# Kernel tuning notes

Hardware: AMD Instinct MI355X
Metric: run time of the kernel (lower is better)

## Reference

```python
import jax, jax.numpy as jnp
import numpy as np

SOS = 4998
EOS = 4999
SCALING = 2.0


def setup_inputs() -> dict:
    key = jax.random.key(0)
    ks = jax.random.split(key, 12)
    B, T, E, D, A, C, F, ODIM, L = 32, 1000, 512, 1024, 512, 10, 100, 5000, 100
    s = 0.02
    return {
        "hpad": jax.random.normal(ks[0], (B, T, E), jnp.float32),
        "ys": jax.random.randint(ks[1], (B, L), 0, SOS, jnp.int32),
        # AttLoc params
        "w_enc": jax.random.normal(ks[2], (A, E), jnp.float32) * s,
        "b_enc": jnp.zeros((A,), jnp.float32),
        "w_dec": jax.random.normal(ks[3], (A, D), jnp.float32) * s,
        "w_att": jax.random.normal(ks[4], (A, C), jnp.float32) * s,
        "w_conv": jax.random.normal(ks[5], (C, 1, 2 * F + 1), jnp.float32) * s,  # OIH 1D conv kernel
        "w_gvec": jax.random.normal(ks[6], (1, A), jnp.float32) * s,
        "b_gvec": jnp.zeros((1,), jnp.float32),
        # Decoder params
        "embed": jax.random.normal(ks[7], (ODIM, D), jnp.float32) * s,
        "w_ih": jax.random.normal(ks[8], (4 * D, D + E), jnp.float32) * s,
        "w_hh": jax.random.normal(ks[9], (4 * D, D), jnp.float32) * s,
        "b_ih": jnp.zeros((4 * D,), jnp.float32),
        "b_hh": jnp.zeros((4 * D,), jnp.float32),
        "w_out": jax.random.normal(ks[10], (ODIM, D), jnp.float32) * s,
        "b_out": jnp.zeros((ODIM,), jnp.float32),
    }


def _decode(hpad, ys, w_enc, b_enc, w_dec, w_att, w_conv, w_gvec, b_gvec,
            embed, w_ih, w_hh, b_ih, b_hh, w_out, b_out):
    B, T, E = hpad.shape
    D = w_hh.shape[1]
    F = (w_conv.shape[-1] - 1) // 2
    # ys_in = [sos; y] per utterance (all same length -> already padded)
    ys_in = jnp.concatenate([jnp.full((B, 1), SOS, ys.dtype), ys], axis=1)  # [B, olen]
    eys = embed[ys_in]                                                      # [B, olen, D]
    # pre_compute_enc_h = mlp_enc(enc_h)
    pre = jnp.einsum('bte,ae->bta', hpad, w_enc) + b_enc                    # [B, T, A]
    att0 = jnp.full((B, T), 1.0 / T, hpad.dtype)   # uniform init attention (all hlen == T)
    z0 = jnp.zeros((B, D), hpad.dtype)
    c0 = jnp.zeros((B, D), hpad.dtype)

    def step(carry, ey_i):
        z, c, aw = carry
        # location-aware conv over previous attention weights: [B,1,T] -> [B,C,T]
        conv = jax.lax.conv_general_dilated(aw[:, None, :], w_conv, (1,), [(F, F)],
                                            dimension_numbers=('NCH', 'OIH', 'NCH'))
        att_feat = jnp.einsum('bct,ac->bta', conv, w_att)                   # mlp_att
        dec = (z @ w_dec.T)[:, None, :]                                     # mlp_dec, tiled
        e = jnp.tanh(att_feat + pre + dec) @ w_gvec[0] + b_gvec[0]          # [B, T]
        w = jax.nn.softmax(SCALING * e, axis=1)
        ctx = jnp.einsum('bt,bte->be', w, hpad)                             # [B, E]
        # LSTMCell
        x = jnp.concatenate([ey_i, ctx], axis=1)                            # [B, D+E]
        gates = x @ w_ih.T + b_ih + z @ w_hh.T + b_hh
        i_g, f_g, g_g, o_g = jnp.split(gates, 4, axis=1)
        c_new = jax.nn.sigmoid(f_g) * c + jax.nn.sigmoid(i_g) * jnp.tanh(g_g)
        z_new = jax.nn.sigmoid(o_g) * jnp.tanh(c_new)
        return (z_new, c_new, w), z_new

    _, z_all = jax.lax.scan(step, (z0, c0, att0), jnp.swapaxes(eys, 0, 1))  # [olen, B, D]
    y_all = jnp.einsum('obd,vd->obv', z_all, w_out) + b_out                 # [olen, B, odim]
    return jnp.swapaxes(y_all, 0, 1)                                        # [B, olen, odim]


def reference(hpad, ys, w_enc, b_enc, w_dec, w_att, w_conv, w_gvec, b_gvec,
              embed, w_ih, w_hh, b_ih, b_hh, w_out, b_out):
    return _decode(hpad, ys, w_enc, b_enc, w_dec, w_att, w_conv, w_gvec, b_gvec,
                   embed, w_ih, w_hh, b_ih, b_hh, w_out, b_out)
```

## Files before the change

kernel.cpp:

```cpp
#include <hip/hip_runtime.h>
#include <math.h>

#define B_    32
#define T_    1000
#define E_    512
#define D_    1024
#define A_    512
#define C_    10
#define F_    100
#define ODIM_ 5000
#define OLEN_ 101
#define SOS_  4998

#define OFF_PRE   0u
#define N_PREF    (32u*512u*1000u/2u)
#define OFF_HPB   (OFF_PRE + N_PREF)
#define N_HPBF    (32u*1000u*512u/2u)
#define OFF_DEC   (OFF_HPB + N_HPBF)
#define N_DEC     (32u*512u)
#define OFF_CONV  (OFF_DEC + N_DEC)
#define N_CONVB   (32u*10u*1000u)
#define OFF_AW    (OFF_CONV + N_CONVB)
#define N_AW      (32u*1000u)
#define OFF_S     (OFF_AW + N_AW)
#define N_S       (64u)
#define OFF_CTX   (OFF_S + N_S)
#define N_CTX     (32u*512u)
#define OFF_GP    (OFF_CTX + N_CTX)
#define N_GP      (8u*32u*4096u)
#define OFF_Z     (OFF_GP + N_GP)
#define N_Z       (32u*1024u)
#define OFF_C     (OFF_Z + N_Z)
#define OFF_ZALL  (OFF_C + N_Z)

__device__ __forceinline__ float fast_tanh(float x) {
    float cx = fminf(8.f, fmaxf(-8.f, x));
    float e = __expf(2.f * cx);
    return (e - 1.f) * __builtin_amdgcn_rcpf(e + 1.f);
}
__device__ __forceinline__ float fast_sigmoid(float x) {
    float cx = fminf(30.f, fmaxf(-30.f, x));
    return __builtin_amdgcn_rcpf(1.f + __expf(-cx));
}

__device__ __forceinline__ unsigned bf16rne(float f) {
    unsigned u = __float_as_uint(f);
    return (u + 0x7fffu + ((u >> 16) & 1u)) >> 16;
}
__device__ __forceinline__ unsigned packbf(float lo, float hi) {
    return bf16rne(lo) | (bf16rne(hi) << 16);
}
__device__ __forceinline__ float bflo(unsigned u) { return __uint_as_float(u << 16); }
__device__ __forceinline__ float bfhi(unsigned u) { return __uint_as_float(u & 0xffff0000u); }

__global__ __launch_bounds__(256) void k_init(float* ws) {
    int i = blockIdx.x * 256 + threadIdx.x;
    if (i < (int)N_Z) { ws[OFF_Z + i] = 0.f; ws[OFF_C + i] = 0.f; }
    if (i < (int)N_CTX) ws[OFF_CTX + i] = 0.f;
    if (i < (int)N_AW) ws[OFF_AW + i] = 1.0f;
    if (i < 64) ws[OFF_S + i] = (i >= 32) ? 1000.f : 0.f;
}

__global__ __launch_bounds__(256) void k_hp16(const float* __restrict__ hp, float* ws) {
    uint2* hpb = (uint2*)(ws + OFF_HPB);
    const float4* src = (const float4*)hp;
    for (unsigned i = blockIdx.x * 256 + threadIdx.x; i < 4096000u; i += 4000u * 256u) {
        float4 v = src[i];
        uint2 o;
        o.x = packbf(v.x, v.y);
        o.y = packbf(v.z, v.w);
        hpb[i] = o;
    }
}

__global__ __launch_bounds__(256) void k_pre_t(const float* __restrict__ hp,
                                               const float* __restrict__ we,
                                               const float* __restrict__ be,
                                               float* ws) {
    __shared__ float As[64][68];
    __shared__ float Bs[64][68];
    unsigned short* preb = (unsigned short*)(ws + OFF_PRE);
    int bt = blockIdx.y;
    int b = bt >> 4, tc = bt & 15;
    int t0 = tc * 64;
    int n0 = blockIdx.x * 64;
    int tid = threadIdx.x;
    int tr = tid >> 4, tcl = tid & 15;
    float acc[4][4] = {};
    for (int k0 = 0; k0 < 512; k0 += 64) {
        for (int i = tid; i < 1024; i += 256) {
            int m = i >> 4, kq = (i & 15) << 2;
            int t = t0 + m;
            float4 v = (t < 1000) ? *(const float4*)&hp[((size_t)(b * 1000 + t)) * 512 + k0 + kq]
                                  : make_float4(0.f, 0.f, 0.f, 0.f);
            As[kq + 0][m] = v.x; As[kq + 1][m] = v.y; As[kq + 2][m] = v.z; As[kq + 3][m] = v.w;
            float4 w = *(const float4*)&we[(size_t)(n0 + m) * 512 + k0 + kq];
            Bs[kq + 0][m] = w.x; Bs[kq + 1][m] = w.y; Bs[kq + 2][m] = w.z; Bs[kq + 3][m] = w.w;
        }
        __syncthreads();
        #pragma unroll 16
        for (int kk = 0; kk < 64; ++kk) {
            float4 av = *(const float4*)&As[kk][tr << 2];
            float4 bv = *(const float4*)&Bs[kk][tcl << 2];
            float a[4] = {av.x, av.y, av.z, av.w};
            float bq[4] = {bv.x, bv.y, bv.z, bv.w};
            #pragma unroll
            for (int i = 0; i < 4; i++)
                #pragma unroll
                for (int j = 0; j < 4; j++) acc[i][j] += a[i] * bq[j];
        }
        __syncthreads();
    }
    int tt = t0 + (tr << 2);
    if (tt < 1000) {
        #pragma unroll
        for (int j = 0; j < 4; ++j) {
            int a = n0 + (tcl << 2) + j;
            float bea = be[a];
            uint2 o;
            o.x = packbf(acc[0][j] + bea, acc[1][j] + bea);
            o.y = packbf(acc[2][j] + bea, acc[3][j] + bea);
            *(uint2*)&preb[((size_t)(b * 512 + a)) * 1000 + tt] = o;
        }
    }
}

__global__ __launch_bounds__(256, 2) void k_prep(const float* __restrict__ wdec,
                                                 const float* __restrict__ wconv,
                                                 const float* __restrict__ wih,
                                                 const float* __restrict__ whh,
                                                 const float* __restrict__ embed,
                                                 const int* __restrict__ ys,
                                                 float* ws, int step) {
    int tid = threadIdx.x;
    if (blockIdx.x < 1024) {
        int u = blockIdx.x;
        if (u < 64) ws[OFF_CTX + u * 256 + tid] = 0.f;
        if (u == 64 && tid < 32) ws[OFF_S + (step & 1) * 32 + tid] = 0.f;
        int w = u * 4 + (tid >> 6);
        int lane = tid & 63;
        int a = w >> 3, bg7 = w & 7;
        const float4* wr = (const float4*)(wdec + (size_t)a * 1024);
        float4 w4[4];
        #pragma unroll
        for (int i = 0; i < 4; i++) w4[i] = wr[i * 64 + lane];
        float acc[4] = {0.f, 0.f, 0.f, 0.f};
        #pragma unroll
        for (int bb = 0; bb < 4; ++bb) {
            const float4* zr = (const float4*)(ws + OFF_Z + (size_t)(bg7 * 4 + bb) * 1024);
            #pragma unroll
            for (int i = 0; i < 4; i++) {
                float4 z4 = zr[i * 64 + lane];
                acc[bb] += w4[i].x * z4.x + w4[i].y * z4.y + w4[i].z * z4.z + w4[i].w * z4.w;
            }
        }
        #pragma unroll
        for (int off = 32; off > 0; off >>= 1) {
            acc[0] += __shfl_xor(acc[0], off, 64);
            acc[1] += __shfl_xor(acc[1], off, 64);
            acc[2] += __shfl_xor(acc[2], off, 64);
            acc[3] += __shfl_xor(acc[3], off, 64);
        }
        if (lane == 0) {
            #pragma unroll
            for (int bb = 0; bb < 4; ++bb)
                ws[OFF_DEC + (bg7 * 4 + bb) * 512 + a] = acc[bb];
        }
    } else if (blockIdx.x < 1344) {
        int blk = blockIdx.x - 1024;
        int b = blk / 10, c = blk - b * 10;
        if (tid >= 250) return;
        float invS = __builtin_amdgcn_rcpf(ws[OFF_S + ((step + 1) & 1) * 32 + b]);
        int t = tid * 4;
        const float* ar = ws + OFF_AW + b * 1000;
        const float* wc = wconv + c * 201;
        float a0, a1, a2, a3;
        a0 = (t - 100 >= 0) ? ar[t - 100] : 0.f;
        a1 = (t -  99 >= 0) ? ar[t -  99] : 0.f;
        a2 = (t -  98 >= 0) ? ar[t -  98] : 0.f;
        a3 = (t -  97 >= 0) ? ar[t -  97] : 0.f;
        float c0 = 0.f, c1 = 0.f, c2 = 0.f, c3 = 0.f;
        #pragma unroll 4
        for (int j = 0; j < 201; ++j) {
            float w = wc[j];
            c0 += a0 * w; c1 += a1 * w; c2 += a2 * w; c3 += a3 * w;
            a0 = a1; a1 = a2; a2 = a3;
            int ni = t + j - 96;
            a3 = (ni >= 0 && ni < 1000) ? ar[ni] : 0.f;
        }
        float* o = ws + OFF_CONV + (size_t)(b * 10 + c) * 1000 + t;
        o[0] = c0 * invS; o[1] = c1 * invS; o[2] = c2 * invS; o[3] = c3 * invS;
    } else {
        __shared__ float wlds[32][132];
        __shared__ float xs[32][36];
        int blk = blockIdx.x - 1344;
        int nt = blk & 31, ks = blk >> 5;
        int n0 = nt * 128;
        bool isE = (ks < 4);
        int kloc = isE ? ks * 256 : (ks - 4) * 256;
        int r = tid >> 1, h = tid & 1;
        int bx = tid >> 3, q8 = tid & 7;
        int tok = (step == 0) ? SOS_ : ys[bx * 100 + step - 1];
        const float* xsrc = isE ? (embed + (size_t)tok * 1024 + kloc)
                                : (ws + OFF_Z + (size_t)bx * 1024 + kloc);
        int nq = tid & 31, bq = tid >> 5;
        float acc[4][4] = {};
        for (int kc = 0; kc < 8; ++kc) {
            int koff = kc * 32;
            {
                const float* wrow = isE ? (wih + (size_t)(n0 + r) * 1536 + kloc + koff + h * 16)
                                        : (whh + (size_t)(n0 + r) * 1024 + kloc + koff + h * 16);
                #pragma unroll
                for (int j = 0; j < 4; ++j) {
                    float4 v = *(const float4*)&wrow[j * 4];
                    int kb = h * 16 + j * 4;
                    wlds[kb + 0][r] = v.x; wlds[kb + 1][r] = v.y;
                    wlds[kb + 2][r] = v.z; wlds[kb + 3][r] = v.w;
                }
            }
            {
                float4 v = *(const float4*)&xsrc[koff + q8 * 4];
                xs[q8 * 4 + 0][bx] = v.x; xs[q8 * 4 + 1][bx] = v.y;
                xs[q8 * 4 + 2][bx] = v.z; xs[q8 * 4 + 3][bx] = v.w;
            }
            __syncthreads();
            #pragma unroll 8
            for (int kk = 0; kk < 32; ++kk) {
                float4 wv = *(const float4*)&wlds[kk][nq * 4];
                float4 xv = *(const float4*)&xs[kk][bq * 4];
                float wa[4] = {wv.x, wv.y, wv.z, wv.w};
                float xa[4] = {xv.x, xv.y, xv.z, xv.w};
                #pragma unroll
                for (int i = 0; i < 4; i++)
                    #pragma unroll
                    for (int j = 0; j < 4; j++) acc[i][j] += wa[i] * xa[j];
            }
            __syncthreads();
        }
        float* gp = ws + OFF_GP + (size_t)(ks * 32 + bq * 4) * 4096 + n0 + nq * 4;
        #pragma unroll
        for (int j = 0; j < 4; j++)
            #pragma unroll
            for (int i = 0; i < 4; i++)
                gp[(size_t)j * 4096 + i] = acc[i][j];
    }
}

__global__ __launch_bounds__(512, 2) void k_ectx(const float* __restrict__ watt,
                                                 const float* __restrict__ gvec,
                                                 const float* __restrict__ bgv,
                                                 float* ws, int step) {
    __shared__ float sa[512 * 12];
    __shared__ float part[1024];
    __shared__ float wsh[128];
    const unsigned short* preb = (const unsigned short*)(ws + OFF_PRE);
    const unsigned short* hpb  = (const unsigned short*)(ws + OFF_HPB);
    int b = blockIdx.x >> 3, tc = blockIdx.x & 7;
    int tbase = tc * 128;
    int tid = threadIdx.x;
    {
        const float* wrow = watt + tid * 10;
        float* d = sa + tid * 12;
        #pragma unroll
        for (int c = 0; c < 10; ++c) d[c] = wrow[c];
        d[10] = gvec[tid];
        d[11] = ws[OFF_DEC + b * 512 + tid];
    }
    __syncthreads();
    int w = tid >> 6, l = tid & 63;
    int t = tbase + l * 2;
    bool valid = (t < 1000);
    float2 cvv[10];
    const float* convb = ws + OFF_CONV + b * 10000;
    #pragma unroll
    for (int c = 0; c < 10; ++c)
        cvv[c] = valid ? *(const float2*)&convb[c * 1000 + t] : make_float2(0.f, 0.f);
    int a0 = w * 64;
    const unsigned short* pt = preb + ((size_t)(b * 512 + a0)) * 1000 + t;
    float ex = 0.f, ey = 0.f;
    #pragma unroll 8
    for (int a = a0; a < a0 + 64; ++a) {
        unsigned u = valid ? *(const unsigned*)pt : 0u;
        pt += 1000;
        const float4* sp = (const float4*)(sa + a * 12);
        float4 w0 = sp[0];
        float4 w1 = sp[1];
        float4 w2 = sp[2];
        float px = bflo(u), py = bfhi(u);
        float sx = px + w2.w, sy = py + w2.w;
        sx += cvv[0].x * w0.x; sy += cvv[0].y * w0.x;
        sx += cvv[1].x * w0.y; sy += cvv[1].y * w0.y;
        sx += cvv[2].x * w0.z; sy += cvv[2].y * w0.z;
        sx += cvv[3].x * w0.w; sy += cvv[3].y * w0.w;
        sx += cvv[4].x * w1.x; sy += cvv[4].y * w1.x;
        sx += cvv[5].x * w1.y; sy += cvv[5].y * w1.y;
        sx += cvv[6].x * w1.z; sy += cvv[6].y * w1.z;
        sx += cvv[7].x * w1.w; sy += cvv[7].y * w1.w;
        sx += cvv[8].x * w2.x; sy += cvv[8].y * w2.x;
        sx += cvv[9].x * w2.y; sy += cvv[9].y * w2.y;
        ex += w2.z * fast_tanh(sx);
        ey += w2.z * fast_tanh(sy);
    }
    part[w * 128 + l * 2]     = ex;
    part[w * 128 + l * 2 + 1] = ey;
    __syncthreads();
    float wtil = 0.f;
    if (tid < 128) {
        int tt = tbase + tid;
        float e = 0.f;
        #pragma unroll
        for (int j = 0; j < 8; ++j) e += part[j * 128 + tid];
        if (tt < 1000) {
            wtil = __expf(2.f * (e + bgv[0]));
            ws[OFF_AW + b * 1000 + tt] = wtil;
        }
        wsh[tid] = wtil;
    }
    __syncthreads();
    part[tid] = wtil;
    __syncthreads();
    for (int off = 256; off >= 1; off >>= 1) {
        if (tid < off) part[tid] += part[tid + off];
        __syncthreads();
    }
    if (tid == 0) atomicAdd(&ws[OFF_S + (step & 1) * 32 + b], part[0]);
    int e4 = tid & 127, th = tid >> 7;
    int lt0 = th * 32;
    int ltend = lt0 + 32;
    int tmax = 1000 - tbase; if (ltend > tmax) ltend = tmax;
    float4 acc = make_float4(0.f, 0.f, 0.f, 0.f);
    for (int lt = lt0; lt < ltend; ++lt) {
        float wv = wsh[lt];
        uint2 hu = *(const uint2*)&hpb[((size_t)(b * 1000 + tbase + lt)) * 512 + e4 * 4];
        acc.x += wv * bflo(hu.x); acc.y += wv * bfhi(hu.x);
        acc.z += wv * bflo(hu.y); acc.w += wv * bfhi(hu.y);
    }
    float* cx = ws + OFF_CTX + b * 512 + e4 * 4;
    atomicAdd(cx + 0, acc.x); atomicAdd(cx + 1, acc.y);
    atomicAdd(cx + 2, acc.z); atomicAdd(cx + 3, acc.w);
}

__global__ __launch_bounds__(256, 2) void k_gl(const float* __restrict__ wih,
                                               const float* __restrict__ bih,
                                               const float* __restrict__ bhh,
                                               float* ws, int step) {
    __shared__ float wlds[32][20];
    __shared__ float xs[32][33];
    __shared__ float glb[16][33];
    __shared__ float sinv[32];
    int tid = threadIdx.x;
    int d0 = blockIdx.x * 4;
    if (tid < 32) sinv[tid] = __builtin_amdgcn_rcpf(ws[OFF_S + (step & 1) * 32 + tid]);
    __syncthreads();
    int r = tid >> 4, h = tid & 15;
    int ng_r = (r >> 2) * 1024 + d0 + (r & 3);
    const float* wrow = wih + (size_t)ng_r * 1536 + 1024 + h * 2;
    int bx = tid >> 3, q8 = tid & 7;
    const float* xsrc = ws + OFF_CTX + (size_t)bx * 512 + q8 * 4;
    float xscale = sinv[bx];
    int nq = tid & 7, bq = tid >> 3;
    float acc[2] = {0.f, 0.f};
    for (int kc = 0; kc < 16; ++kc) {
        int k0 = kc * 32;
        {
            float2 v = *(const float2*)&wrow[k0];
            wlds[h * 2 + 0][r] = v.x;
            wlds[h * 2 + 1][r] = v.y;
        }
        {
            float4 v = *(const float4*)&xsrc[k0];
            xs[q8 * 4 + 0][bx] = v.x * xscale; xs[q8 * 4 + 1][bx] = v.y * xscale;
            xs[q8 * 4 + 2][bx] = v.z * xscale; xs[q8 * 4 + 3][bx] = v.w * xscale;
        }
        __syncthreads();
        #pragma unroll 8
        for (int kk = 0; kk < 32; ++kk) {
            float w0 = wlds[kk][nq * 2], w1 = wlds[kk][nq * 2 + 1];
            float x  = xs[kk][bq];
            acc[0] += w0 * x;
            acc[1] += w1 * x;
        }
        __syncthreads();
    }
    #pragma unroll
    for (int i = 0; i < 2; ++i) {
        int nl = nq * 2 + i;
        int ng = (nl >> 2) * 1024 + d0 + (nl & 3);
        float s = acc[i] + bih[ng] + bhh[ng];
        #pragma unroll
        for (int sl = 0; sl < 8; ++sl)
            s += ws[OFF_GP + (size_t)(sl * 32 + bq) * 4096 + ng];
        glb[nl][bq] = s;
    }
    __syncthreads();
    if (tid < 128) {
        int dl = tid >> 5, b = tid & 31;
        float gi = glb[dl][b];
        float gf = glb[4 + dl][b];
        float gg = glb[8 + dl][b];
        float go = glb[12 + dl][b];
        int id = b * 1024 + d0 + dl;
        float c_old = ws[OFF_C + id];
        float si = fast_sigmoid(gi);
        float sf = fast_sigmoid(gf);
        float so = fast_sigmoid(go);
        float cn = sf * c_old + si * fast_tanh(gg);
        float hh = so * fast_tanh(cn);
        ws[OFF_C + id] = cn;
        ws[OFF_Z + id] = hh;
        ws[OFF_ZALL + ((size_t)step * 32 + b) * 1024 + d0 + dl] = hh;
    }
}

__global__ __launch_bounds__(256) void k_out(const float* __restrict__ zall,
                                             const float* __restrict__ wo,
                                             const float* __restrict__ bo,
                                             float* __restrict__ out) {
    __shared__ float As[64][68];
    __shared__ float Bs[64][68];
    int m0 = blockIdx.y * 64, n0 = blockIdx.x * 64;
    int tid = threadIdx.x;
    int tr = tid >> 4, tc = tid & 15;
    float acc[4][4] = {};
    for (int k0 = 0; k0 < 1024; k0 += 64) {
        for (int i = tid; i < 1024; i += 256) {
            int m = i >> 4, kq = (i & 15) << 2;
            int gm = m0 + m;
            float4 v = (gm < 3232) ? *(const float4*)&zall[(size_t)gm * 1024 + k0 + kq]
                                   : make_float4(0.f, 0.f, 0.f, 0.f);
            As[kq + 0][m] = v.x; As[kq + 1][m] = v.y; As[kq + 2][m] = v.z; As[kq + 3][m] = v.w;
            int gn = n0 + m;
            float4 w = (gn < 5000) ? *(const float4*)&wo[(size_t)gn * 1024 + k0 + kq]
                                   : make_float4(0.f, 0.f, 0.f, 0.f);
            Bs[kq + 0][m] = w.x; Bs[kq + 1][m] = w.y; Bs[kq + 2][m] = w.z; Bs[kq + 3][m] = w.w;
        }
        __syncthreads();
        #pragma unroll 16
        for (int kk = 0; kk < 64; ++kk) {
            float4 av = *(const float4*)&As[kk][tr << 2];
            float4 bv = *(const float4*)&Bs[kk][tc << 2];
            float a[4] = {av.x, av.y, av.z, av.w};
            float b[4] = {bv.x, bv.y, bv.z, bv.w};
            #pragma unroll
            for (int i = 0; i < 4; i++)
                #pragma unroll
                for (int j = 0; j < 4; j++) acc[i][j] += a[i] * b[j];
        }
        __syncthreads();
    }
    #pragma unroll
    for (int i = 0; i < 4; i++) {
        int m = m0 + (tr << 2) + i;
        if (m >= 3232) continue;
        int b = m & 31, o = m >> 5;
        #pragma unroll
        for (int j = 0; j < 4; j++) {
            int v = n0 + (tc << 2) + j;
            if (v < 5000)
                out[((size_t)b * 101 + o) * 5000 + v] = acc[i][j] + bo[v];
        }
    }
}

extern "C" void kernel_launch(void* const* d_in, const int* in_sizes, int n_in,
                              void* d_out, int out_size, void* d_ws, size_t ws_size,
                              hipStream_t stream) {
    const float* hpad   = (const float*)d_in[0];
    const int*   ys     = (const int*)d_in[1];
    const float* w_enc  = (const float*)d_in[2];
    const float* b_enc  = (const float*)d_in[3];
    const float* w_dec  = (const float*)d_in[4];
    const float* w_att  = (const float*)d_in[5];
    const float* w_conv = (const float*)d_in[6];
    const float* w_gvec = (const float*)d_in[7];
    const float* b_gvec = (const float*)d_in[8];
    const float* embed  = (const float*)d_in[9];
    const float* w_ih   = (const float*)d_in[10];
    const float* w_hh   = (const float*)d_in[11];
    const float* b_ih   = (const float*)d_in[12];
    const float* b_hh   = (const float*)d_in[13];
    const float* w_out  = (const float*)d_in[14];
    const float* b_out  = (const float*)d_in[15];
    float* ws  = (float*)d_ws;
    float* out = (float*)d_out;

    k_init<<<128, 256, 0, stream>>>(ws);
    k_hp16<<<4000, 256, 0, stream>>>(hpad, ws);
    k_pre_t<<<dim3(8, 512), 256, 0, stream>>>(hpad, w_enc, b_enc, ws);

    for (int step = 0; step < OLEN_; ++step) {
        k_prep<<<1600, 256, 0, stream>>>(w_dec, w_conv, w_ih, w_hh, embed, ys, ws, step);
        k_ectx<<<256, 512, 0, stream>>>(w_att, w_gvec, b_gvec, ws, step);
        k_gl<<<256, 256, 0, stream>>>(w_ih, b_ih, b_hh, ws, step);
    }

    k_out<<<dim3(79, 51), 256, 0, stream>>>(ws + OFF_ZALL, w_out, b_out, out);
}
```

Measured before the change: 10.19 ms.

## Fuse LSTM gate GEMMs into k_gl, double-buffer z, retile output GEMM

Moves the embedding and recurrent-state gate partial products out of k_prep and into k_gl, which now computes all gate contributions over the full K=2560 in one pass. This drops the partial-sum buffer and its eight-way readback. The hidden state z is double-buffered so k_prep can read the previous step while k_gl writes the next. The attention-sum reduction in k_ectx uses wave shuffles instead of an LDS tree. The final vocab projection uses 128x128 tiles with an 8x8 per-thread micro-tile. The trade-off is that k_gl carries more serial K work per block, while k_prep loses its parallel GEMM blocks.

After: 19.24 ms. +88.9%, slower.

```diff
diff --git a/kernel.cpp b/kernel.cpp
--- a/kernel.cpp
+++ b/kernel.cpp
@@ -26,12 +26,10 @@
 #define N_S       (64u)
 #define OFF_CTX   (OFF_S + N_S)
 #define N_CTX     (32u*512u)
-#define OFF_GP    (OFF_CTX + N_CTX)
-#define N_GP      (8u*32u*4096u)
-#define OFF_Z     (OFF_GP + N_GP)
-#define N_Z       (32u*1024u)
-#define OFF_C     (OFF_Z + N_Z)
-#define OFF_ZALL  (OFF_C + N_Z)
+#define OFF_Z     (OFF_CTX + N_CTX)
+#define N_Z1      (32u*1024u)
+#define OFF_C     (OFF_Z + 2u*N_Z1)
+#define OFF_ZALL  (OFF_C + N_Z1)
 
 __device__ __forceinline__ float fast_tanh(float x) {
     float cx = fminf(8.f, fmaxf(-8.f, x));
@@ -55,7 +53,7 @@
 
 __global__ __launch_bounds__(256) void k_init(float* ws) {
     int i = blockIdx.x * 256 + threadIdx.x;
-    if (i < (int)N_Z) { ws[OFF_Z + i] = 0.f; ws[OFF_C + i] = 0.f; }
+    if (i < (int)N_Z1) { ws[OFF_Z + i] = 0.f; ws[OFF_C + i] = 0.f; }
     if (i < (int)N_CTX) ws[OFF_CTX + i] = 0.f;
     if (i < (int)N_AW) ws[OFF_AW + i] = 1.0f;
     if (i < 64) ws[OFF_S + i] = (i >= 32) ? 1000.f : 0.f;
@@ -127,10 +125,6 @@
 
 __global__ __launch_bounds__(256, 2) void k_prep(const float* __restrict__ wdec,
                                                  const float* __restrict__ wconv,
-                                                 const float* __restrict__ wih,
-                                                 const float* __restrict__ whh,
-                                                 const float* __restrict__ embed,
-                                                 const int* __restrict__ ys,
                                                  float* ws, int step) {
     int tid = threadIdx.x;
     if (blockIdx.x < 1024) {
@@ -140,6 +134,7 @@
         int w = u * 4 + (tid >> 6);
         int lane = tid & 63;
         int a = w >> 3, bg7 = w & 7;
+        const float* zin = ws + OFF_Z + (step & 1) * N_Z1;
         const float4* wr = (const float4*)(wdec + (size_t)a * 1024);
         float4 w4[4];
         #pragma unroll
@@ -147,7 +142,7 @@
         float acc[4] = {0.f, 0.f, 0.f, 0.f};
         #pragma unroll
         for (int bb = 0; bb < 4; ++bb) {
-            const float4* zr = (const float4*)(ws + OFF_Z + (size_t)(bg7 * 4 + bb) * 1024);
+            const float4* zr = (const float4*)(zin + (size_t)(bg7 * 4 + bb) * 1024);
             #pragma unroll
             for (int i = 0; i < 4; i++) {
                 float4 z4 = zr[i * 64 + lane];
@@ -166,7 +161,7 @@
             for (int bb = 0; bb < 4; ++bb)
                 ws[OFF_DEC + (bg7 * 4 + bb) * 512 + a] = acc[bb];
         }
-    } else if (blockIdx.x < 1344) {
+    } else {
         int blk = blockIdx.x - 1024;
         int b = blk / 10, c = blk - b * 10;
         if (tid >= 250) return;
@@ -190,59 +185,6 @@
         }
         float* o = ws + OFF_CONV + (size_t)(b * 10 + c) * 1000 + t;
         o[0] = c0 * invS; o[1] = c1 * invS; o[2] = c2 * invS; o[3] = c3 * invS;
-    } else {
-        __shared__ float wlds[32][132];
-        __shared__ float xs[32][36];
-        int blk = blockIdx.x - 1344;
-        int nt = blk & 31, ks = blk >> 5;
-        int n0 = nt * 128;
-        bool isE = (ks < 4);
-        int kloc = isE ? ks * 256 : (ks - 4) * 256;
-        int r = tid >> 1, h = tid & 1;
-        int bx = tid >> 3, q8 = tid & 7;
-        int tok = (step == 0) ? SOS_ : ys[bx * 100 + step - 1];
-        const float* xsrc = isE ? (embed + (size_t)tok * 1024 + kloc)
-                                : (ws + OFF_Z + (size_t)bx * 1024 + kloc);
-        int nq = tid & 31, bq = tid >> 5;
-        float acc[4][4] = {};
-        for (int kc = 0; kc < 8; ++kc) {
-            int koff = kc * 32;
-            {
-                const float* wrow = isE ? (wih + (size_t)(n0 + r) * 1536 + kloc + koff + h * 16)
-                                        : (whh + (size_t)(n0 + r) * 1024 + kloc + koff + h * 16);
-                #pragma unroll
-                for (int j = 0; j < 4; ++j) {
-                    float4 v = *(const float4*)&wrow[j * 4];
-                    int kb = h * 16 + j * 4;
-                    wlds[kb + 0][r] = v.x; wlds[kb + 1][r] = v.y;
-                    wlds[kb + 2][r] = v.z; wlds[kb + 3][r] = v.w;
-                }
-            }
-            {
-                float4 v = *(const float4*)&xsrc[koff + q8 * 4];
-                xs[q8 * 4 + 0][bx] = v.x; xs[q8 * 4 + 1][bx] = v.y;
-                xs[q8 * 4 + 2][bx] = v.z; xs[q8 * 4 + 3][bx] = v.w;
-            }
-            __syncthreads();
-            #pragma unroll 8
-            for (int kk = 0; kk < 32; ++kk) {
-                float4 wv = *(const float4*)&wlds[kk][nq * 4];
-                float4 xv = *(const float4*)&xs[kk][bq * 4];
-                float wa[4] = {wv.x, wv.y, wv.z, wv.w};
-                float xa[4] = {xv.x, xv.y, xv.z, xv.w};
-                #pragma unroll
-                for (int i = 0; i < 4; i++)
-                    #pragma unroll
-                    for (int j = 0; j < 4; j++) acc[i][j] += wa[i] * xa[j];
-            }
-            __syncthreads();
-        }
-        float* gp = ws + OFF_GP + (size_t)(ks * 32 + bq * 4) * 4096 + n0 + nq * 4;
-        #pragma unroll
-        for (int j = 0; j < 4; j++)
-            #pragma unroll
-            for (int i = 0; i < 4; i++)
-                gp[(size_t)j * 4096 + i] = acc[i][j];
     }
 }
 
@@ -317,13 +259,14 @@
         wsh[tid] = wtil;
     }
     __syncthreads();
-    part[tid] = wtil;
-    __syncthreads();
-    for (int off = 256; off >= 1; off >>= 1) {
-        if (tid < off) part[tid] += part[tid + off];
-        __syncthreads();
-    }
-    if (tid == 0) atomicAdd(&ws[OFF_S + (step & 1) * 32 + b], part[0]);
+    if (tid < 128) {
+        float ss = wtil;
+        #pragma unroll
+        for (int off = 32; off > 0; off >>= 1) ss += __shfl_xor(ss, off, 64);
+        if ((tid & 63) == 0) part[tid >> 6] = ss;
+    }
+    __syncthreads();
+    if (tid == 0) atomicAdd(&ws[OFF_S + (step & 1) * 32 + b], part[0] + part[1]);
     int e4 = tid & 127, th = tid >> 7;
     int lt0 = th * 32;
     int ltend = lt0 + 32;
@@ -341,56 +284,77 @@
 }
 
 __global__ __launch_bounds__(256, 2) void k_gl(const float* __restrict__ wih,
+                                               const float* __restrict__ whh,
+                                               const float* __restrict__ embed,
+                                               const int* __restrict__ ys,
                                                const float* __restrict__ bih,
                                                const float* __restrict__ bhh,
                                                float* ws, int step) {
-    __shared__ float wlds[32][20];
-    __shared__ float xs[32][33];
+    __shared__ float wlds[64][17];
+    __shared__ float xs[64][33];
     __shared__ float glb[16][33];
     __shared__ float sinv[32];
+    __shared__ int   toks[32];
     int tid = threadIdx.x;
     int d0 = blockIdx.x * 4;
-    if (tid < 32) sinv[tid] = __builtin_amdgcn_rcpf(ws[OFF_S + (step & 1) * 32 + tid]);
-    __syncthreads();
-    int r = tid >> 4, h = tid & 15;
+    if (tid < 32) {
+        sinv[tid] = __builtin_amdgcn_rcpf(ws[OFF_S + (step & 1) * 32 + tid]);
+        toks[tid] = (step == 0) ? SOS_ : ys[tid * 100 + step - 1];
+    }
+    __syncthreads();
+    int r = tid >> 4, kq4 = (tid & 15) * 4;
     int ng_r = (r >> 2) * 1024 + d0 + (r & 3);
-    const float* wrow = wih + (size_t)ng_r * 1536 + 1024 + h * 2;
-    int bx = tid >> 3, q8 = tid & 7;
-    const float* xsrc = ws + OFF_CTX + (size_t)bx * 512 + q8 * 4;
+    int bx = tid >> 3, kq8 = (tid & 7) * 8;
     float xscale = sinv[bx];
+    int tok = toks[bx];
+    const float* zin = ws + OFF_Z + (step & 1) * N_Z1;
     int nq = tid & 7, bq = tid >> 3;
-    float acc[2] = {0.f, 0.f};
-    for (int kc = 0; kc < 16; ++kc) {
-        int k0 = kc * 32;
+    float acc0 = 0.f, acc1 = 0.f;
+    for (int kc = 0; kc < 40; ++kc) {
+        int k0 = kc * 64;
         {
-            float2 v = *(const float2*)&wrow[k0];
-            wlds[h * 2 + 0][r] = v.x;
-            wlds[h * 2 + 1][r] = v.y;
+            const float* wsrc = (k0 < 1536)
+                ? (wih + (size_t)ng_r * 1536 + k0 + kq4)
+                : (whh + (size_t)ng_r * 1024 + (k0 - 1536) + kq4);
+            float4 wv = *(const float4*)wsrc;
+            wlds[kq4 + 0][r] = wv.x; wlds[kq4 + 1][r] = wv.y;
+            wlds[kq4 + 2][r] = wv.z; wlds[kq4 + 3][r] = wv.w;
         }
         {
-            float4 v = *(const float4*)&xsrc[k0];
-            xs[q8 * 4 + 0][bx] = v.x * xscale; xs[q8 * 4 + 1][bx] = v.y * xscale;
-            xs[q8 * 4 + 2][bx] = v.z * xscale; xs[q8 * 4 + 3][bx] = v.w * xscale;
-        }
-        __syncthreads();
-        #pragma unroll 8
-        for (int kk = 0; kk < 32; ++kk) {
+            float4 v0, v1;
+            float sc = 1.f;
+            if (k0 < 1024) {
+                const float* s = embed + (size_t)tok * 1024 + k0 + kq8;
+                v0 = ((const float4*)s)[0]; v1 = ((const float4*)s)[1];
+            } else if (k0 < 1536) {
+                const float* s = ws + OFF_CTX + (size_t)bx * 512 + (k0 - 1024) + kq8;
+                v0 = ((const float4*)s)[0]; v1 = ((const float4*)s)[1];
+                sc = xscale;
+            } else {
+                const float* s = zin + (size_t)bx * 1024 + (k0 - 1536) + kq8;
+                v0 = ((const float4*)s)[0]; v1 = ((const float4*)s)[1];
+            }
+            xs[kq8 + 0][bx] = v0.x * sc; xs[kq8 + 1][bx] = v0.y * sc;
+            xs[kq8 + 2][bx] = v0.z * sc; xs[kq8 + 3][bx] = v0.w * sc;
+            xs[kq8 + 4][bx] = v1.x * sc; xs[kq8 + 5][bx] = v1.y * sc;
+            xs[kq8 + 6][bx] = v1.z * sc; xs[kq8 + 7][bx] = v1.w * sc;
+        }
+        __syncthreads();
+        #pragma unroll 16
+        for (int kk = 0; kk < 64; ++kk) {
             float w0 = wlds[kk][nq * 2], w1 = wlds[kk][nq * 2 + 1];
             float x  = xs[kk][bq];
-            acc[0] += w0 * x;
-            acc[1] += w1 * x;
-        }
-        __syncthreads();
-    }
-    #pragma unroll
-    for (int i = 0; i < 2; ++i) {
-        int nl = nq * 2 + i;
-        int ng = (nl >> 2) * 1024 + d0 + (nl & 3);
-        float s = acc[i] + bih[ng] + bhh[ng];
-        #pragma unroll
-        for (int sl = 0; sl < 8; ++sl)
-            s += ws[OFF_GP + (size_t)(sl * 32 + bq) * 4096 + ng];
-        glb[nl][bq] = s;
+            acc0 += w0 * x;
+            acc1 += w1 * x;
+        }
+        __syncthreads();
+    }
+    {
+        int nl0 = nq * 2, nl1 = nq * 2 + 1;
+        int ng0 = (nl0 >> 2) * 1024 + d0 + (nl0 & 3);
+        int ng1 = (nl1 >> 2) * 1024 + d0 + (nl1 & 3);
+        glb[nl0][bq] = acc0 + bih[ng0] + bhh[ng0];
+        glb[nl1][bq] = acc1 + bih[ng1] + bhh[ng1];
     }
     __syncthreads();
     if (tid < 128) {
@@ -399,15 +363,15 @@
         float gf = glb[4 + dl][b];
         float gg = glb[8 + dl][b];
         float go = glb[12 + dl][b];
-        int id = b * 1024 + d0 + dl;
-        float c_old = ws[OFF_C + id];
+        int idl = b * 1024 + d0 + dl;
+        float c_old = ws[OFF_C + idl];
         float si = fast_sigmoid(gi);
         float sf = fast_sigmoid(gf);
         float so = fast_sigmoid(go);
         float cn = sf * c_old + si * fast_tanh(gg);
         float hh = so * fast_tanh(cn);
-        ws[OFF_C + id] = cn;
-        ws[OFF_Z + id] = hh;
+        ws[OFF_C + idl] = cn;
+        ws[OFF_Z + ((step + 1) & 1) * N_Z1 + idl] = hh;
         ws[OFF_ZALL + ((size_t)step * 32 + b) * 1024 + d0 + dl] = hh;
     }
 }
@@ -416,46 +380,56 @@
                                              const float* __restrict__ wo,
                                              const float* __restrict__ bo,
                                              float* __restrict__ out) {
-    __shared__ float As[64][68];
-    __shared__ float Bs[64][68];
-    int m0 = blockIdx.y * 64, n0 = blockIdx.x * 64;
+    __shared__ float As[16][132];
+    __shared__ float Bs[16][132];
+    int m0 = blockIdx.y * 128, n0 = blockIdx.x * 128;
     int tid = threadIdx.x;
-    int tr = tid >> 4, tc = tid & 15;
-    float acc[4][4] = {};
-    for (int k0 = 0; k0 < 1024; k0 += 64) {
-        for (int i = tid; i < 1024; i += 256) {
-            int m = i >> 4, kq = (i & 15) << 2;
-            int gm = m0 + m;
-            float4 v = (gm < 3232) ? *(const float4*)&zall[(size_t)gm * 1024 + k0 + kq]
-                                   : make_float4(0.f, 0.f, 0.f, 0.f);
-            As[kq + 0][m] = v.x; As[kq + 1][m] = v.y; As[kq + 2][m] = v.z; As[kq + 3][m] = v.w;
-            int gn = n0 + m;
-            float4 w = (gn < 5000) ? *(const float4*)&wo[(size_t)gn * 1024 + k0 + kq]
-                                   : make_float4(0.f, 0.f, 0.f, 0.f);
-            Bs[kq + 0][m] = w.x; Bs[kq + 1][m] = w.y; Bs[kq + 2][m] = w.z; Bs[kq + 3][m] = w.w;
-        }
-        __syncthreads();
-        #pragma unroll 16
-        for (int kk = 0; kk < 64; ++kk) {
-            float4 av = *(const float4*)&As[kk][tr << 2];
-            float4 bv = *(const float4*)&Bs[kk][tc << 2];
-            float a[4] = {av.x, av.y, av.z, av.w};
-            float b[4] = {bv.x, bv.y, bv.z, bv.w};
+    int tx = tid & 15, ty = tid >> 4;
+    float acc[8][8] = {};
+    int ar = tid >> 1, ah = (tid & 1) * 8;
+    for (int k0 = 0; k0 < 1024; k0 += 16) {
+        {
+            int gm = m0 + ar;
+            float4 a0, a1;
+            if (gm < 3232) {
+                a0 = *(const float4*)&zall[(size_t)gm * 1024 + k0 + ah];
+                a1 = *(const float4*)&zall[(size_t)gm * 1024 + k0 + ah + 4];
+            } else { a0 = a1 = make_float4(0.f, 0.f, 0.f, 0.f); }
+            As[ah + 0][ar] = a0.x; As[ah + 1][ar] = a0.y; As[ah + 2][ar] = a0.z; As[ah + 3][ar] = a0.w;
+            As[ah + 4][ar] = a1.x; As[ah + 5][ar] = a1.y; As[ah + 6][ar] = a1.z; As[ah + 7][ar] = a1.w;
+            int gn = n0 + ar;
+            float4 b0, b1;
+            if (gn < 5000) {
+                b0 = *(const float4*)&wo[(size_t)gn * 1024 + k0 + ah];
+                b1 = *(const float4*)&wo[(size_t)gn * 1024 + k0 + ah + 4];
+            } else { b0 = b1 = make_float4(0.f, 0.f, 0.f, 0.f); }
+            Bs[ah + 0][ar] = b0.x; Bs[ah + 1][ar] = b0.y; Bs[ah + 2][ar] = b0.z; Bs[ah + 3][ar] = b0.w;
+            Bs[ah + 4][ar] = b1.x; Bs[ah + 5][ar] = b1.y; Bs[ah + 6][ar] = b1.z; Bs[ah + 7][ar] = b1.w;
+        }
+        __syncthreads();
+        #pragma unroll
+        for (int kk = 0; kk < 16; ++kk) {
+            float4 a0v = *(const float4*)&As[kk][ty * 8];
+            float4 a1v = *(const float4*)&As[kk][ty * 8 + 4];
+            float4 b0v = *(const float4*)&Bs[kk][tx * 8];
+            float4 b1v = *(const float4*)&Bs[kk][tx * 8 + 4];
+            float am[8] = {a0v.x, a0v.y, a0v.z, a0v.w, a1v.x, a1v.y, a1v.z, a1v.w};
+            float bn[8] = {b0v.x, b0v.y, b0v.z, b0v.w, b1v.x, b1v.y, b1v.z, b1v.w};
             #pragma unroll
-            for (int i = 0; i < 4; i++)
+            for (int i = 0; i < 8; i++)
                 #pragma unroll
-                for (int j = 0; j < 4; j++) acc[i][j] += a[i] * b[j];
+                for (int j = 0; j < 8; j++) acc[i][j] += am[i] * bn[j];
         }
         __syncthreads();
     }
     #pragma unroll
-    for (int i = 0; i < 4; i++) {
-        int m = m0 + (tr << 2) + i;
+    for (int i = 0; i < 8; i++) {
+        int m = m0 + ty * 8 + i;
         if (m >= 3232) continue;
         int b = m & 31, o = m >> 5;
         #pragma unroll
-        for (int j = 0; j < 4; j++) {
-            int v = n0 + (tc << 2) + j;
+        for (int j = 0; j < 8; j++) {
+            int v = n0 + tx * 8 + j;
             if (v < 5000)
                 out[((size_t)b * 101 + o) * 5000 + v] = acc[i][j] + bo[v];
         }
@@ -489,10 +463,10 @@
     k_pre_t<<<dim3(8, 512), 256, 0, stream>>>(hpad, w_enc, b_enc, ws);
 
     for (int step = 0; step < OLEN_; ++step) {
-        k_prep<<<1600, 256, 0, stream>>>(w_dec, w_conv, w_ih, w_hh, embed, ys, ws, step);
+        k_prep<<<1344, 256, 0, stream>>>(w_dec, w_conv, ws, step);
         k_ectx<<<256, 512, 0, stream>>>(w_att, w_gvec, b_gvec, ws, step);
-        k_gl<<<256, 256, 0, stream>>>(w_ih, b_ih, b_hh, ws, step);
-    }
-
-    k_out<<<dim3(79, 51), 256, 0, stream>>>(ws + OFF_ZALL, w_out, b_out, out);
-}
+        k_gl<<<256, 256, 0, stream>>>(w_ih, w_hh, embed, ys, b_ih, b_hh, ws, step);
+    }
+
+    k_out<<<dim3(40, 26), 256, 0, stream>>>(ws + OFF_ZALL, w_out, b_out, out);
+}
```
